# Kernel tuning notes

Measured on AMD Instinct MI355X. Metric: run time of the kernel, lower is better.

Reference implementation:

```python
import jax, jax.numpy as jnp
import numpy as np

B, S, D, H = 2, 2048, 1024, 16
DH = D // H
NEG = jnp.float32(-1e30)


def setup_inputs() -> dict:
    key = jax.random.key(0)
    ks = jax.random.split(key, 5)
    x = jax.random.normal(ks[0], (B, S, D), dtype=jnp.float32)
    # causal mask: attn_mask == 0 means blocked (matches masked_fill(attn_mask == 0))
    attn_mask = jnp.tril(jnp.ones((S, S), dtype=jnp.int32))
    key_padding_mask = jnp.zeros((B, S), dtype=bool)  # True = pad (none here)
    sd = 1.0 / np.sqrt(D)
    W_qkv = jax.random.normal(ks[1], (D, 3 * D), dtype=jnp.float32) * sd
    b_qkv = jnp.zeros((3 * D,), dtype=jnp.float32)
    W_proj = jax.random.normal(ks[2], (D, D), dtype=jnp.float32) * sd
    b_proj = jnp.zeros((D,), dtype=jnp.float32)
    return {"x": x, "W_qkv": W_qkv, "b_qkv": b_qkv, "W_proj": W_proj,
            "b_proj": b_proj, "attn_mask": attn_mask,
            "key_padding_mask": key_padding_mask}


def reference(x, W_qkv, b_qkv, W_proj, b_proj, attn_mask, key_padding_mask):
    scale = jnp.float32(DH) ** -0.5
    qkv = (x @ W_qkv + b_qkv).reshape(B, S, 3, H, DH)
    qkv = jnp.transpose(qkv, (2, 0, 3, 1, 4))  # (3, B, H, S, DH)
    q, k, v = qkv[0], qkv[1], qkv[2]
    attn = jnp.einsum("bhqd,bhkd->bhqk", q, k) * scale  # (B,H,S,S)
    # key padding mask: True -> -inf on that key column
    attn = jnp.where(key_padding_mask[:, None, None, :], NEG, attn)
    # attn mask: 0 -> blocked
    attn = jnp.where(attn_mask[None, None, :, :] == 0, NEG, attn)
    attn = jax.nn.softmax(attn, axis=-1)
    out = jnp.einsum("bhqk,bhkd->bhqd", attn, v)
    out = jnp.transpose(out, (0, 2, 1, 3)).reshape(B, S, D)
    return out @ W_proj + b_proj
```

## Files before the change

kernel.cpp:

```cpp
#include <hip/hip_runtime.h>


typedef __bf16 bf16;
typedef bf16 bf16x4 __attribute__((ext_vector_type(4)));
typedef bf16 bf16x8 __attribute__((ext_vector_type(8)));
typedef float f32x4 __attribute__((ext_vector_type(4)));

#define S_LEN 2048
#define DMODEL 1024
#define NHEAD 16
#define DHEAD 64

__device__ __forceinline__ void async_ld16(void* lds, const void* g) {
  __builtin_amdgcn_global_load_lds(
      (const __attribute__((address_space(1))) unsigned int*)g,
      (__attribute__((address_space(3))) unsigned int*)lds, 16, 0, 0);
}

__global__ __launch_bounds__(256) void prep_kernel(
    const float* __restrict__ x, const float* __restrict__ Wq,
    const float* __restrict__ Wp, bf16* __restrict__ Xb,
    bf16* __restrict__ Wtq, bf16* __restrict__ Wtp) {
  __shared__ float t[32][33];
  const int bid = blockIdx.x, tid = threadIdx.x;
  if (bid < 4096) {
    int i = bid * 256 + tid;
    float4 v = ((const float4*)x)[i];
    bf16x4 o;
    o[0] = (bf16)v.x; o[1] = (bf16)v.y; o[2] = (bf16)v.z; o[3] = (bf16)v.w;
    *(bf16x4*)(&Xb[4 * i]) = o;
    return;
  }
  const float* in; bf16* out; int R, C, bx, by;
  if (bid < 7168) {
    int b = bid - 4096; in = Wq; out = Wtq; R = 1024; C = 3072;
    bx = b % 96; by = b / 96;
  } else {
    int b = bid - 7168; in = Wp; out = Wtp; R = 1024; C = 1024;
    bx = b % 32; by = b / 32;
  }
  int tx = tid & 31, ty = tid >> 5;
  int bc = bx * 32, br = by * 32;
#pragma unroll
  for (int i = 0; i < 32; i += 8)
    t[ty + i][tx] = in[(size_t)(br + ty + i) * C + bc + tx];
  __syncthreads();
#pragma unroll
  for (int i = 0; i < 32; i += 8)
    out[(size_t)(bc + ty + i) * R + br + tx] = (bf16)t[tx][ty + i];
}

__global__ __launch_bounds__(512) void gemm_qkv(
    const bf16* __restrict__ A, const bf16* __restrict__ Bt,
    const float* __restrict__ bias, bf16* __restrict__ Oq,
    bf16* __restrict__ Ok, bf16* __restrict__ Ov, int Ksz) {
  __shared__ bf16 As[256 * 32];
  __shared__ bf16 Bs[128 * 32];
  const int tid = threadIdx.x, lane = tid & 63, w = tid >> 6;
  const int wm = (w >> 1) * 64, wn = (w & 1) * 64;
  const int lr = lane & 15, kg = lane >> 4;
  const int m0 = blockIdx.y * 256, n0 = blockIdx.x * 128;

  f32x4 acc[4][4] = {};

  bf16x8 areg[2], breg;
  const int ar0 = (tid) >> 2,        ac0 = (tid & 3) * 8;
  const int ar1 = (tid + 512) >> 2,  ac1 = ((tid + 512) & 3) * 8;
  const int br_ = tid >> 2,          bc_ = (tid & 3) * 8;

  areg[0] = *(const bf16x8*)(&A[(size_t)(m0 + ar0) * Ksz + ac0]);
  areg[1] = *(const bf16x8*)(&A[(size_t)(m0 + ar1) * Ksz + ac1]);
  breg    = *(const bf16x8*)(&Bt[(size_t)(n0 + br_) * Ksz + bc_]);

  for (int k0 = 0; k0 < Ksz; k0 += 32) {
    *(bf16x8*)(&As[ar0 * 32 + ac0]) = areg[0];
    *(bf16x8*)(&As[ar1 * 32 + ac1]) = areg[1];
    *(bf16x8*)(&Bs[br_ * 32 + bc_]) = breg;
    __syncthreads();

    if (k0 + 32 < Ksz) {
      const int kn = k0 + 32;
      areg[0] = *(const bf16x8*)(&A[(size_t)(m0 + ar0) * Ksz + kn + ac0]);
      areg[1] = *(const bf16x8*)(&A[(size_t)(m0 + ar1) * Ksz + kn + ac1]);
      breg    = *(const bf16x8*)(&Bt[(size_t)(n0 + br_) * Ksz + kn + bc_]);
    }

    bf16x8 af[4], bfr[4];
#pragma unroll
    for (int i = 0; i < 4; ++i)
      af[i] = *(const bf16x8*)(&As[(wm + i * 16 + lr) * 32 + kg * 8]);
#pragma unroll
    for (int j = 0; j < 4; ++j)
      bfr[j] = *(const bf16x8*)(&Bs[(wn + j * 16 + lr) * 32 + kg * 8]);
#pragma unroll
    for (int i = 0; i < 4; ++i)
#pragma unroll
      for (int j = 0; j < 4; ++j)
        acc[i][j] = __builtin_amdgcn_mfma_f32_16x16x32_bf16(af[i], bfr[j], acc[i][j], 0, 0, 0);
    __syncthreads();
  }

  const int rbase = kg * 4;
  const int t = n0 >> 10;
  if (t == 2) {
#pragma unroll
    for (int i = 0; i < 4; ++i) {
#pragma unroll
      for (int j = 0; j < 4; ++j) {
        int ncol = n0 + wn + j * 16 + lr;
        float bv = bias[ncol];
        int rem = ncol & 1023, h = rem >> 6, d = rem & 63;
        int m = m0 + wm + i * 16 + rbase;
        int s = m & 2047;
        size_t hb = (size_t)((m >> 11) * NHEAD + h) * S_LEN;
        bf16x4 pk;
#pragma unroll
        for (int r = 0; r < 4; ++r) pk[r] = (bf16)(acc[i][j][r] + bv);
        *(bf16x4*)(&Ov[hb * DHEAD + (size_t)d * S_LEN + s]) = pk;
      }
    }
  } else {
    bf16* Oqk = (t == 0) ? Oq : Ok;
#pragma unroll
    for (int i = 0; i < 4; ++i) {
#pragma unroll
      for (int j = 0; j < 4; ++j) {
        int ncol = n0 + wn + j * 16 + lr;
        float bv = bias[ncol];
        int rem = ncol & 1023, h = rem >> 6, d = rem & 63;
#pragma unroll
        for (int r = 0; r < 4; ++r) {
          int m = m0 + wm + i * 16 + rbase + r;
          int s = m & 2047;
          size_t hb = (size_t)((m >> 11) * NHEAD + h) * S_LEN;
          Oqk[(hb + s) * DHEAD + d] = (bf16)(acc[i][j][r] + bv);
        }
      }
    }
  }
}

__global__ __launch_bounds__(256) void gemm_proj(
    const bf16* __restrict__ A, const bf16* __restrict__ Bt,
    const float* __restrict__ bias, float* __restrict__ Of,
    int Ksz, int Nsz) {
  __shared__ bf16 As[64 * 32];
  __shared__ bf16 Bs[128 * 32];
  const int tid = threadIdx.x, lane = tid & 63, w = tid >> 6;
  const int wm = (w >> 1) * 32, wn = (w & 1) * 64;
  const int lr = lane & 15, kg = lane >> 4;
  const int m0 = blockIdx.y * 64, n0 = blockIdx.x * 128;

  f32x4 acc[2][4] = {};

  bf16x8 areg, breg[2];
  const int ar_ = tid >> 2,          ac_ = (tid & 3) * 8;
  const int br0 = tid >> 2,          bc0 = (tid & 3) * 8;
  const int br1 = (tid + 256) >> 2,  bc1 = ((tid + 256) & 3) * 8;

  areg    = *(const bf16x8*)(&A[(size_t)(m0 + ar_) * Ksz + ac_]);
  breg[0] = *(const bf16x8*)(&Bt[(size_t)(n0 + br0) * Ksz + bc0]);
  breg[1] = *(const bf16x8*)(&Bt[(size_t)(n0 + br1) * Ksz + bc1]);

  for (int k0 = 0; k0 < Ksz; k0 += 32) {
    *(bf16x8*)(&As[ar_ * 32 + ac_]) = areg;
    *(bf16x8*)(&Bs[br0 * 32 + bc0]) = breg[0];
    *(bf16x8*)(&Bs[br1 * 32 + bc1]) = breg[1];
    __syncthreads();

    if (k0 + 32 < Ksz) {
      const int kn = k0 + 32;
      areg    = *(const bf16x8*)(&A[(size_t)(m0 + ar_) * Ksz + kn + ac_]);
      breg[0] = *(const bf16x8*)(&Bt[(size_t)(n0 + br0) * Ksz + kn + bc0]);
      breg[1] = *(const bf16x8*)(&Bt[(size_t)(n0 + br1) * Ksz + kn + bc1]);
    }

    bf16x8 af[2], bfr[4];
#pragma unroll
    for (int i = 0; i < 2; ++i)
      af[i] = *(const bf16x8*)(&As[(wm + i * 16 + lr) * 32 + kg * 8]);
#pragma unroll
    for (int j = 0; j < 4; ++j)
      bfr[j] = *(const bf16x8*)(&Bs[(wn + j * 16 + lr) * 32 + kg * 8]);
#pragma unroll
    for (int i = 0; i < 2; ++i)
#pragma unroll
      for (int j = 0; j < 4; ++j)
        acc[i][j] = __builtin_amdgcn_mfma_f32_16x16x32_bf16(af[i], bfr[j], acc[i][j], 0, 0, 0);
    __syncthreads();
  }

  const int rbase = kg * 4;
#pragma unroll
  for (int i = 0; i < 2; ++i) {
#pragma unroll
    for (int j = 0; j < 4; ++j) {
      int ncol = n0 + wn + j * 16 + lr;
      float bv = bias[ncol];
#pragma unroll
      for (int r = 0; r < 4; ++r) {
        int m = m0 + wm + i * 16 + rbase + r;
        Of[(size_t)m * Nsz + ncol] = acc[i][j][r] + bv;
      }
    }
  }
}

__global__ __launch_bounds__(256) void attn_kernel(
    const bf16* __restrict__ Q, const bf16* __restrict__ K,
    const bf16* __restrict__ Vtg, bf16* __restrict__ O) {
  __shared__ bf16 Ks[128 * 72];
  __shared__ bf16 Vt[80 * 136];
  __shared__ bf16 Pt[4][16 * 136];

  const int tid = threadIdx.x, lane = tid & 63, w = tid >> 6;
  const int lr = lane & 15, quad = lane >> 4;
  const int flat = blockIdx.x;
  const int p = (flat >> 3) & 15;
  const int bh = (flat & 7) + ((flat >> 7) << 3);
  const int b = bh >> 4, h = bh & 15;
  const bf16* Qp = Q + (size_t)bh * S_LEN * DHEAD;
  const bf16* Kp = K + (size_t)bh * S_LEN * DHEAD;
  const bf16* Vp = Vtg + (size_t)bh * S_LEN * DHEAD;

  for (int i = tid; i < 16 * 136; i += 256) {
    int rr = i / 136;
    Vt[(64 + rr) * 136 + (i - rr * 136)] = (rr == 0) ? (bf16)1.0f : (bf16)0.0f;
  }
  __syncthreads();

  const float qs = 0.125f * 1.44269504f;

  for (int seg = 0; seg < 2; ++seg) {
    const int qt = seg ? (31 - p) : p;
    const int q0 = qt * 64;
    const int qrow = q0 + w * 16;

    bf16x8 q0r = *(const bf16x8*)(Qp + (size_t)(qrow + lr) * DHEAD + quad * 8);
    bf16x8 q1r = *(const bf16x8*)(Qp + (size_t)(qrow + lr) * DHEAD + 32 + quad * 8);
    bf16x8 qf0, qf1;
#pragma unroll
    for (int e = 0; e < 8; ++e) {
      qf0[e] = (bf16)((float)q0r[e] * qs);
      qf1[e] = (bf16)((float)q1r[e] * qs);
    }

    f32x4 acc[4] = {};
    f32x4 acc5 = {};
    float m_i = -1e30f;

    const int ktiles = (q0 + 63) / 128 + 1;

    bf16x8 kreg[4], vreg[4];
#pragma unroll
    for (int i = 0; i < 4; ++i) {
      int sg = tid + i * 256;
      int krow = sg >> 3, kc = (sg & 7) * 8;
      kreg[i] = *(const bf16x8*)(&Kp[(size_t)krow * DHEAD + kc]);
      int vd = sg >> 4, vs = (sg & 15) * 8;
      vreg[i] = *(const bf16x8*)(&Vp[(size_t)vd * S_LEN + vs]);
    }

    for (int kt = 0; kt < ktiles; ++kt) {
      const int kb = kt * 128;
#pragma unroll
      for (int i = 0; i < 4; ++i) {
        int sg = tid + i * 256;
        int krow = sg >> 3, kc = (sg & 7) * 8;
        *(bf16x8*)(&Ks[krow * 72 + kc]) = kreg[i];
        int vd = sg >> 4, vs = (sg & 15) * 8;
        *(bf16x8*)(&Vt[vd * 136 + vs]) = vreg[i];
      }
      __syncthreads();

      if (kt + 1 < ktiles) {
        const int kbn = kb + 128;
#pragma unroll
        for (int i = 0; i < 4; ++i) {
          int sg = tid + i * 256;
          int krow = sg >> 3, kc = (sg & 7) * 8;
          kreg[i] = *(const bf16x8*)(&Kp[(size_t)(kbn + krow) * DHEAD + kc]);
          int vd = sg >> 4, vs = (sg & 15) * 8;
          vreg[i] = *(const bf16x8*)(&Vp[(size_t)vd * S_LEN + kbn + vs]);
        }
      }

      f32x4 sc[8];
      __builtin_amdgcn_s_setprio(1);
#pragma unroll
      for (int ct = 0; ct < 8; ++ct) {
        bf16x8 kf0 = *(const bf16x8*)(&Ks[(ct * 16 + lr) * 72 + quad * 8]);
        bf16x8 kf1 = *(const bf16x8*)(&Ks[(ct * 16 + lr) * 72 + 32 + quad * 8]);
        f32x4 a = {};
        a = __builtin_amdgcn_mfma_f32_16x16x32_bf16(kf0, qf0, a, 0, 0, 0);
        a = __builtin_amdgcn_mfma_f32_16x16x32_bf16(kf1, qf1, a, 0, 0, 0);
        sc[ct] = a;
      }
      __builtin_amdgcn_s_setprio(0);

      const bool full = (kb + 127) <= qrow;
      float pmax = -1e30f;
      if (full) {
#pragma unroll
        for (int ct = 0; ct < 8; ++ct)
#pragma unroll
          for (int r = 0; r < 4; ++r) pmax = fmaxf(pmax, sc[ct][r]);
      } else {
        const int qg = qrow + lr;
#pragma unroll
        for (int ct = 0; ct < 8; ++ct)
#pragma unroll
          for (int r = 0; r < 4; ++r) {
            int key = kb + ct * 16 + quad * 4 + r;
            if (key > qg) sc[ct][r] = -1e30f;
            pmax = fmaxf(pmax, sc[ct][r]);
          }
      }
      pmax = fmaxf(pmax, __shfl_xor(pmax, 16));
      pmax = fmaxf(pmax, __shfl_xor(pmax, 32));

      if (!__all(pmax <= m_i + 8.0f)) {
        float mn = fmaxf(m_i, pmax);
        float alpha = __builtin_amdgcn_exp2f(m_i - mn);
        m_i = mn;
#pragma unroll
        for (int nt = 0; nt < 4; ++nt)
#pragma unroll
          for (int r = 0; r < 4; ++r) acc[nt][r] *= alpha;
#pragma unroll
        for (int r = 0; r < 4; ++r) acc5[r] *= alpha;
      }

#pragma unroll
      for (int ct = 0; ct < 8; ++ct)
#pragma unroll
        for (int r = 0; r < 4; ++r)
          sc[ct][r] = __builtin_amdgcn_exp2f(sc[ct][r] - m_i);

#pragma unroll
      for (int ct = 0; ct < 8; ++ct) {
        bf16x4 pk;
#pragma unroll
        for (int r = 0; r < 4; ++r) pk[r] = (bf16)sc[ct][r];
        *(bf16x4*)(&Pt[w][lr * 136 + ct * 16 + quad * 4]) = pk;
      }

      __builtin_amdgcn_s_setprio(1);
#pragma unroll
      for (int k0 = 0; k0 < 4; ++k0) {
        bf16x8 pf = *(const bf16x8*)(&Pt[w][lr * 136 + k0 * 32 + quad * 8]);
#pragma unroll
        for (int nt = 0; nt < 4; ++nt) {
          bf16x8 vf = *(const bf16x8*)(&Vt[(nt * 16 + lr) * 136 + k0 * 32 + quad * 8]);
          acc[nt] = __builtin_amdgcn_mfma_f32_16x16x32_bf16(vf, pf, acc[nt], 0, 0, 0);
        }
        bf16x8 vf5 = *(const bf16x8*)(&Vt[(64 + lr) * 136 + k0 * 32 + quad * 8]);
        acc5 = __builtin_amdgcn_mfma_f32_16x16x32_bf16(vf5, pf, acc5, 0, 0, 0);
      }
      __builtin_amdgcn_s_setprio(0);
      __syncthreads();
    }

    float lsum = __shfl(acc5[0], lr);
    float inv = 1.f / lsum;
    size_t base = ((size_t)(b * S_LEN + qrow + lr)) * DMODEL + h * DHEAD;
#pragma unroll
    for (int nt = 0; nt < 4; ++nt) {
      bf16x4 ov;
#pragma unroll
      for (int r = 0; r < 4; ++r) ov[r] = (bf16)(acc[nt][r] * inv);
      *(bf16x4*)(&O[base + nt * 16 + quad * 4]) = ov;
    }
  }
}

extern "C" void kernel_launch(void* const* d_in, const int* in_sizes, int n_in,
                              void* d_out, int out_size, void* d_ws, size_t ws_size,
                              hipStream_t stream) {
  (void)in_sizes; (void)n_in; (void)out_size; (void)ws_size;
  const float* x     = (const float*)d_in[0];
  const float* Wqkv  = (const float*)d_in[1];
  const float* bqkv  = (const float*)d_in[2];
  const float* Wproj = (const float*)d_in[3];
  const float* bproj = (const float*)d_in[4];
  float* out = (float*)d_out;

  char* ws = (char*)d_ws;
  bf16* Xb  = (bf16*)(ws + 0);
  bf16* AO  = (bf16*)(ws + 0);
  bf16* Wtq = (bf16*)(ws + 8388608);
  bf16* Wtp = (bf16*)(ws + 16777216);
  bf16* Qb  = (bf16*)(ws + 18874368);
  bf16* Kb  = (bf16*)(ws + 27262976);
  bf16* Vtg = (bf16*)(ws + 35651584);

  prep_kernel<<<8192, 256, 0, stream>>>(x, Wqkv, Wproj, Xb, Wtq, Wtp);
  gemm_qkv<<<dim3(24, 16), 512, 0, stream>>>(Xb, Wtq, bqkv, Qb, Kb, Vtg, 1024);
  attn_kernel<<<512, 256, 0, stream>>>(Qb, Kb, Vtg, AO);
  gemm_proj<<<dim3(8, 64), 256, 0, stream>>>(AO, Wtp, bproj, out, 1024, 1024);
}
```

Measured before the change: 197.4 us.

## Keep softmax probabilities in registers via permuted K rows, one q-tile per block

Stores K rows in LDS in a permuted order so the QK^T MFMA output layout lines up with the B-operand layout of the PV MFMA. The exponentiated scores can then be packed straight into bf16x8 registers, which removes the per-wave Pt LDS staging buffer and its write/read round trip. The causal mask key index is recomputed to match the permutation. The grid is doubled to one q-tile per block with a four-way balanced tile ordering and a launch-bounds hint of 4 blocks, trading the old paired-segment load balancing for more parallelism and lower LDS use.

```diff
diff --git a/kernel.cpp b/kernel.cpp
--- a/kernel.cpp
+++ b/kernel.cpp
@@ -206,18 +206,19 @@
   }
 }
 
-__global__ __launch_bounds__(256) void attn_kernel(
+__global__ __launch_bounds__(256, 4) void attn_kernel(
     const bf16* __restrict__ Q, const bf16* __restrict__ K,
     const bf16* __restrict__ Vtg, bf16* __restrict__ O) {
   __shared__ bf16 Ks[128 * 72];
   __shared__ bf16 Vt[80 * 136];
-  __shared__ bf16 Pt[4][16 * 136];
 
   const int tid = threadIdx.x, lane = tid & 63, w = tid >> 6;
   const int lr = lane & 15, quad = lane >> 4;
   const int flat = blockIdx.x;
-  const int p = (flat >> 3) & 15;
-  const int bh = (flat & 7) + ((flat >> 7) << 3);
+  const int g = (flat >> 3) & 3, t = flat >> 5;
+  const int bh = (flat & 7) + 8 * g;
+  const int qt = (g == 0) ? t : (g == 1) ? (31 - t)
+               : (g == 2) ? ((t + 16) & 31) : ((15 - t) & 31);
   const int b = bh >> 4, h = bh & 15;
   const bf16* Qp = Q + (size_t)bh * S_LEN * DHEAD;
   const bf16* Kp = K + (size_t)bh * S_LEN * DHEAD;
@@ -230,147 +231,142 @@
   __syncthreads();
 
   const float qs = 0.125f * 1.44269504f;
-
-  for (int seg = 0; seg < 2; ++seg) {
-    const int qt = seg ? (31 - p) : p;
-    const int q0 = qt * 64;
-    const int qrow = q0 + w * 16;
-
-    bf16x8 q0r = *(const bf16x8*)(Qp + (size_t)(qrow + lr) * DHEAD + quad * 8);
-    bf16x8 q1r = *(const bf16x8*)(Qp + (size_t)(qrow + lr) * DHEAD + 32 + quad * 8);
-    bf16x8 qf0, qf1;
-#pragma unroll
-    for (int e = 0; e < 8; ++e) {
-      qf0[e] = (bf16)((float)q0r[e] * qs);
-      qf1[e] = (bf16)((float)q1r[e] * qs);
-    }
-
-    f32x4 acc[4] = {};
-    f32x4 acc5 = {};
-    float m_i = -1e30f;
-
-    const int ktiles = (q0 + 63) / 128 + 1;
-
-    bf16x8 kreg[4], vreg[4];
+  const int q0 = qt * 64;
+  const int qrow = q0 + w * 16;
+
+  bf16x8 q0r = *(const bf16x8*)(Qp + (size_t)(qrow + lr) * DHEAD + quad * 8);
+  bf16x8 q1r = *(const bf16x8*)(Qp + (size_t)(qrow + lr) * DHEAD + 32 + quad * 8);
+  bf16x8 qf0, qf1;
+#pragma unroll
+  for (int e = 0; e < 8; ++e) {
+    qf0[e] = (bf16)((float)q0r[e] * qs);
+    qf1[e] = (bf16)((float)q1r[e] * qs);
+  }
+
+  f32x4 acc[4] = {};
+  f32x4 acc5 = {};
+  float m_i = -1e30f;
+
+  const int ktiles = (q0 + 63) / 128 + 1;
+
+  bf16x8 kreg[4], vreg[4];
+#pragma unroll
+  for (int i = 0; i < 4; ++i) {
+    int sg = tid + i * 256;
+    int krow = sg >> 3, kc = (sg & 7) * 8;
+    kreg[i] = *(const bf16x8*)(&Kp[(size_t)krow * DHEAD + kc]);
+    int vd = sg >> 4, vs = (sg & 15) * 8;
+    vreg[i] = *(const bf16x8*)(&Vp[(size_t)vd * S_LEN + vs]);
+  }
+
+  for (int kt = 0; kt < ktiles; ++kt) {
+    const int kb = kt * 128;
 #pragma unroll
     for (int i = 0; i < 4; ++i) {
       int sg = tid + i * 256;
       int krow = sg >> 3, kc = (sg & 7) * 8;
-      kreg[i] = *(const bf16x8*)(&Kp[(size_t)krow * DHEAD + kc]);
+      int kl = krow & 31;
+      int Rrow = (krow & ~31) | (((kl >> 2) & 1) << 4) | (((kl >> 3) & 3) << 2) | (kl & 3);
+      *(bf16x8*)(&Ks[Rrow * 72 + kc]) = kreg[i];
       int vd = sg >> 4, vs = (sg & 15) * 8;
-      vreg[i] = *(const bf16x8*)(&Vp[(size_t)vd * S_LEN + vs]);
-    }
-
-    for (int kt = 0; kt < ktiles; ++kt) {
-      const int kb = kt * 128;
+      *(bf16x8*)(&Vt[vd * 136 + vs]) = vreg[i];
+    }
+    __syncthreads();
+
+    if (kt + 1 < ktiles) {
+      const int kbn = kb + 128;
 #pragma unroll
       for (int i = 0; i < 4; ++i) {
         int sg = tid + i * 256;
         int krow = sg >> 3, kc = (sg & 7) * 8;
-        *(bf16x8*)(&Ks[krow * 72 + kc]) = kreg[i];
+        kreg[i] = *(const bf16x8*)(&Kp[(size_t)(kbn + krow) * DHEAD + kc]);
         int vd = sg >> 4, vs = (sg & 15) * 8;
-        *(bf16x8*)(&Vt[vd * 136 + vs]) = vreg[i];
-      }
-      __syncthreads();
-
-      if (kt + 1 < ktiles) {
-        const int kbn = kb + 128;
-#pragma unroll
-        for (int i = 0; i < 4; ++i) {
-          int sg = tid + i * 256;
-          int krow = sg >> 3, kc = (sg & 7) * 8;
-          kreg[i] = *(const bf16x8*)(&Kp[(size_t)(kbn + krow) * DHEAD + kc]);
-          int vd = sg >> 4, vs = (sg & 15) * 8;
-          vreg[i] = *(const bf16x8*)(&Vp[(size_t)vd * S_LEN + kbn + vs]);
+        vreg[i] = *(const bf16x8*)(&Vp[(size_t)vd * S_LEN + kbn + vs]);
+      }
+    }
+
+    f32x4 sc[8];
+    __builtin_amdgcn_s_setprio(1);
+#pragma unroll
+    for (int ct = 0; ct < 8; ++ct) {
+      bf16x8 kf0 = *(const bf16x8*)(&Ks[(ct * 16 + lr) * 72 + quad * 8]);
+      bf16x8 kf1 = *(const bf16x8*)(&Ks[(ct * 16 + lr) * 72 + 32 + quad * 8]);
+      f32x4 a = {};
+      a = __builtin_amdgcn_mfma_f32_16x16x32_bf16(kf0, qf0, a, 0, 0, 0);
+      a = __builtin_amdgcn_mfma_f32_16x16x32_bf16(kf1, qf1, a, 0, 0, 0);
+      sc[ct] = a;
+    }
+    __builtin_amdgcn_s_setprio(0);
+
+    const bool full = (kb + 127) <= qrow;
+    float pmax = -1e30f;
+    if (full) {
+#pragma unroll
+      for (int ct = 0; ct < 8; ++ct)
+#pragma unroll
+        for (int r = 0; r < 4; ++r) pmax = fmaxf(pmax, sc[ct][r]);
+    } else {
+      const int qg = qrow + lr;
+#pragma unroll
+      for (int ct = 0; ct < 8; ++ct)
+#pragma unroll
+        for (int r = 0; r < 4; ++r) {
+          int key = kb + (ct >> 1) * 32 + quad * 8 + (ct & 1) * 4 + r;
+          if (key > qg) sc[ct][r] = -1e30f;
+          pmax = fmaxf(pmax, sc[ct][r]);
         }
-      }
-
-      f32x4 sc[8];
-      __builtin_amdgcn_s_setprio(1);
-#pragma unroll
-      for (int ct = 0; ct < 8; ++ct) {
-        bf16x8 kf0 = *(const bf16x8*)(&Ks[(ct * 16 + lr) * 72 + quad * 8]);
-        bf16x8 kf1 = *(const bf16x8*)(&Ks[(ct * 16 + lr) * 72 + 32 + quad * 8]);
-        f32x4 a = {};
-        a = __builtin_amdgcn_mfma_f32_16x16x32_bf16(kf0, qf0, a, 0, 0, 0);
-        a = __builtin_amdgcn_mfma_f32_16x16x32_bf16(kf1, qf1, a, 0, 0, 0);
-        sc[ct] = a;
-      }
-      __builtin_amdgcn_s_setprio(0);
-
-      const bool full = (kb + 127) <= qrow;
-      float pmax = -1e30f;
-      if (full) {
-#pragma unroll
-        for (int ct = 0; ct < 8; ++ct)
-#pragma unroll
-          for (int r = 0; r < 4; ++r) pmax = fmaxf(pmax, sc[ct][r]);
-      } else {
-        const int qg = qrow + lr;
-#pragma unroll
-        for (int ct = 0; ct < 8; ++ct)
-#pragma unroll
-          for (int r = 0; r < 4; ++r) {
-            int key = kb + ct * 16 + quad * 4 + r;
-            if (key > qg) sc[ct][r] = -1e30f;
-            pmax = fmaxf(pmax, sc[ct][r]);
-          }
-      }
-      pmax = fmaxf(pmax, __shfl_xor(pmax, 16));
-      pmax = fmaxf(pmax, __shfl_xor(pmax, 32));
-
-      if (!__all(pmax <= m_i + 8.0f)) {
-        float mn = fmaxf(m_i, pmax);
-        float alpha = __builtin_amdgcn_exp2f(m_i - mn);
-        m_i = mn;
-#pragma unroll
-        for (int nt = 0; nt < 4; ++nt)
-#pragma unroll
-          for (int r = 0; r < 4; ++r) acc[nt][r] *= alpha;
-#pragma unroll
-        for (int r = 0; r < 4; ++r) acc5[r] *= alpha;
-      }
-
-#pragma unroll
-      for (int ct = 0; ct < 8; ++ct)
+    }
+    pmax = fmaxf(pmax, __shfl_xor(pmax, 16));
+    pmax = fmaxf(pmax, __shfl_xor(pmax, 32));
+
+    if (!__all(pmax <= m_i + 8.0f)) {
+      float mn = fmaxf(m_i, pmax);
+      float alpha = __builtin_amdgcn_exp2f(m_i - mn);
+      m_i = mn;
+#pragma unroll
+      for (int nt = 0; nt < 4; ++nt)
+#pragma unroll
+        for (int r = 0; r < 4; ++r) acc[nt][r] *= alpha;
+#pragma unroll
+      for (int r = 0; r < 4; ++r) acc5[r] *= alpha;
+    }
+
+    bf16x8 p8[4];
+#pragma unroll
+    for (int k0 = 0; k0 < 4; ++k0) {
+      bf16x8 pf;
+#pragma unroll
+      for (int c = 0; c < 2; ++c)
 #pragma unroll
         for (int r = 0; r < 4; ++r)
-          sc[ct][r] = __builtin_amdgcn_exp2f(sc[ct][r] - m_i);
-
-#pragma unroll
-      for (int ct = 0; ct < 8; ++ct) {
-        bf16x4 pk;
-#pragma unroll
-        for (int r = 0; r < 4; ++r) pk[r] = (bf16)sc[ct][r];
-        *(bf16x4*)(&Pt[w][lr * 136 + ct * 16 + quad * 4]) = pk;
-      }
-
-      __builtin_amdgcn_s_setprio(1);
-#pragma unroll
-      for (int k0 = 0; k0 < 4; ++k0) {
-        bf16x8 pf = *(const bf16x8*)(&Pt[w][lr * 136 + k0 * 32 + quad * 8]);
-#pragma unroll
-        for (int nt = 0; nt < 4; ++nt) {
-          bf16x8 vf = *(const bf16x8*)(&Vt[(nt * 16 + lr) * 136 + k0 * 32 + quad * 8]);
-          acc[nt] = __builtin_amdgcn_mfma_f32_16x16x32_bf16(vf, pf, acc[nt], 0, 0, 0);
-        }
-        bf16x8 vf5 = *(const bf16x8*)(&Vt[(64 + lr) * 136 + k0 * 32 + quad * 8]);
-        acc5 = __builtin_amdgcn_mfma_f32_16x16x32_bf16(vf5, pf, acc5, 0, 0, 0);
-      }
-      __builtin_amdgcn_s_setprio(0);
-      __syncthreads();
-    }
-
-    float lsum = __shfl(acc5[0], lr);
-    float inv = 1.f / lsum;
-    size_t base = ((size_t)(b * S_LEN + qrow + lr)) * DMODEL + h * DHEAD;
-#pragma unroll
-    for (int nt = 0; nt < 4; ++nt) {
-      bf16x4 ov;
-#pragma unroll
-      for (int r = 0; r < 4; ++r) ov[r] = (bf16)(acc[nt][r] * inv);
-      *(bf16x4*)(&O[base + nt * 16 + quad * 4]) = ov;
-    }
+          pf[c * 4 + r] = (bf16)__builtin_amdgcn_exp2f(sc[2 * k0 + c][r] - m_i);
+      p8[k0] = pf;
+    }
+
+    __builtin_amdgcn_s_setprio(1);
+#pragma unroll
+    for (int k0 = 0; k0 < 4; ++k0) {
+#pragma unroll
+      for (int nt = 0; nt < 4; ++nt) {
+        bf16x8 vf = *(const bf16x8*)(&Vt[(nt * 16 + lr) * 136 + k0 * 32 + quad * 8]);
+        acc[nt] = __builtin_amdgcn_mfma_f32_16x16x32_bf16(vf, p8[k0], acc[nt], 0, 0, 0);
+      }
+      bf16x8 vf5 = *(const bf16x8*)(&Vt[(64 + lr) * 136 + k0 * 32 + quad * 8]);
+      acc5 = __builtin_amdgcn_mfma_f32_16x16x32_bf16(vf5, p8[k0], acc5, 0, 0, 0);
+    }
+    __builtin_amdgcn_s_setprio(0);
+    __syncthreads();
+  }
+
+  float lsum = __shfl(acc5[0], lr);
+  float inv = 1.f / lsum;
+  size_t base = ((size_t)(b * S_LEN + qrow + lr)) * DMODEL + h * DHEAD;
+#pragma unroll
+  for (int nt = 0; nt < 4; ++nt) {
+    bf16x4 ov;
+#pragma unroll
+    for (int r = 0; r < 4; ++r) ov[r] = (bf16)(acc[nt][r] * inv);
+    *(bf16x4*)(&O[base + nt * 16 + quad * 4]) = ov;
   }
 }
 
@@ -396,6 +392,6 @@
 
   prep_kernel<<<8192, 256, 0, stream>>>(x, Wqkv, Wproj, Xb, Wtq, Wtp);
   gemm_qkv<<<dim3(24, 16), 512, 0, stream>>>(Xb, Wtq, bqkv, Qb, Kb, Vtg, 1024);
-  attn_kernel<<<512, 256, 0, stream>>>(Qb, Kb, Vtg, AO);
+  attn_kernel<<<1024, 256, 0, stream>>>(Qb, Kb, Vtg, AO);
   gemm_proj<<<dim3(8, 64), 256, 0, stream>>>(AO, Wtp, bproj, out, 1024, 1024);
 }
```

Result: slower. 207.2 us (+5.0%).
